# Kernel tuning notes

Measured on AMD Instinct MI355X. Metric: run time of the kernel, lower is better.

The kernel has to match this reference:

```python
import jax, jax.numpy as jnp
import numpy as np

N_NODES = 50000
N_EDGES = 1600000
IN_FEAT = 256
OUT_FEAT = 64


def setup_inputs() -> dict:
    key = jax.random.key(0)
    k1, k2, k3, k4, k5, k6 = jax.random.split(key, 6)
    feat = jax.random.normal(k1, (N_NODES, IN_FEAT), dtype=jnp.float32)
    edge_src = jax.random.randint(k2, (N_EDGES,), 0, N_NODES, dtype=jnp.int32)
    edge_dst = jax.random.randint(k3, (N_EDGES,), 0, N_NODES, dtype=jnp.int32)
    edge_weight = jax.random.uniform(k4, (N_EDGES,), dtype=jnp.float32)
    # Xavier-uniform init as in reset_parameters
    bound = float(np.sqrt(6.0 / (IN_FEAT + OUT_FEAT)))
    W_self = jax.random.uniform(k5, (IN_FEAT, OUT_FEAT), minval=-bound, maxval=bound, dtype=jnp.float32)
    W_neigh = jax.random.uniform(k6, (IN_FEAT, OUT_FEAT), minval=-bound, maxval=bound, dtype=jnp.float32)
    return {"feat": feat, "edge_src": edge_src, "edge_dst": edge_dst,
            "edge_weight": edge_weight, "W_self": W_self, "W_neigh": W_neigh}


def reference(feat, edge_src, edge_dst, edge_weight, W_self, W_neigh):
    # neigh_feat = spmm(adj, feat): row dst aggregates weighted neighbors src
    gathered = feat[edge_src] * edge_weight[:, None]          # [E, in_feat]
    neigh_feat = jax.ops.segment_sum(gathered, edge_dst, num_segments=N_NODES)  # [N, in_feat]
    self_feat = feat @ W_self                                 # [N, out_feat]
    neigh_feat = neigh_feat @ W_neigh                         # [N, out_feat]
    out = jax.nn.relu(self_feat + neigh_feat)
    # dropout p=0.0 -> identity
    return out
```

## Files before the change

### kernel.cpp

```cpp
#include <hip/hip_runtime.h>

#define IN_FEAT 256
#define OUT_FEAT 64
#define BBITS 5
#define BSZ 32
#define CAP_SLICE 256
#define CAP_BUCKET 1600
#define CNT_STRIDE 16

typedef __attribute__((ext_vector_type(8))) short bf16x8;
typedef __attribute__((ext_vector_type(4))) float f32x4;

static __device__ __forceinline__ short f2bf(float f) {
    unsigned u = __float_as_uint(f);
    unsigned r = (u + 0x7FFFu + ((u >> 16) & 1u)) >> 16;
    return (short)r;
}
static __device__ __forceinline__ float bflo(unsigned v) {
    return __uint_as_float(v << 16);
}
static __device__ __forceinline__ float bfhi(unsigned v) {
    return __uint_as_float(v & 0xFFFF0000u);
}

__global__ __launch_bounds__(256) void prep(
    const float* __restrict__ Wself,
    const float* __restrict__ Wneigh,
    bf16x8* __restrict__ Wfrag,
    int* __restrict__ cnt, int cnt_words)
{
    const int t = blockIdx.x * 256 + threadIdx.x;
    if (t < 4096) {
        const int kstep = t >> 9;
        const int ntile = (t >> 6) & 7;
        const int lane  = t & 63;
        const int quad  = lane >> 4;
        const int n     = ntile * 16 + (lane & 15);
        const float* src = (n < OUT_FEAT) ? (Wself + n) : (Wneigh + (n - OUT_FEAT));
        const int k0 = kstep * 32 + quad * 8;
        bf16x8 v;
#pragma unroll
        for (int j = 0; j < 8; ++j) v[j] = f2bf(src[(size_t)(k0 + j) * OUT_FEAT]);
        Wfrag[t] = v;
    }
    const int nthr = gridDim.x * 256;
    for (int i = t; i < cnt_words; i += nthr) cnt[i] = 0;
}

__global__ __launch_bounds__(256) void gemm_scatter(
    const float* __restrict__ feat,
    const bf16x8* __restrict__ Wfrag,
    unsigned short* __restrict__ accSelf,
    unsigned short* __restrict__ Pn,
    const int* __restrict__ esrc,
    const int* __restrict__ edst,
    const float* __restrict__ ew,
    int* __restrict__ cnt,
    unsigned* __restrict__ binned,
    int n_nodes, int n_edges, int NB)
{
    const int wave = threadIdx.x >> 6;
    const int lane = threadIdx.x & 63;

    if (wave == 0) {
        const int row0 = blockIdx.x * 16;
        if (row0 < n_nodes) {
            const int quad = lane >> 4;
            const int l15  = lane & 15;

            f32x4 c[8];
#pragma unroll
            for (int i = 0; i < 8; ++i) c[i] = (f32x4){0.f, 0.f, 0.f, 0.f};

            const int arow = min(row0 + l15, n_nodes - 1);
            const float* afeat = feat + (size_t)arow * IN_FEAT + quad * 8;

#pragma unroll
            for (int kstep = 0; kstep < 8; ++kstep) {
                const float4 x = *(const float4*)(afeat + kstep * 32);
                const float4 y = *(const float4*)(afeat + kstep * 32 + 4);
                bf16x8 a;
                a[0] = f2bf(x.x); a[1] = f2bf(x.y); a[2] = f2bf(x.z); a[3] = f2bf(x.w);
                a[4] = f2bf(y.x); a[5] = f2bf(y.y); a[6] = f2bf(y.z); a[7] = f2bf(y.w);
                bf16x8 b[8];
#pragma unroll
                for (int nt = 0; nt < 8; ++nt) b[nt] = Wfrag[(kstep * 8 + nt) * 64 + lane];
#pragma unroll
                for (int nt = 0; nt < 8; ++nt)
                    c[nt] = __builtin_amdgcn_mfma_f32_16x16x32_bf16(a, b[nt], c[nt], 0, 0, 0);
            }

#pragma unroll
            for (int nt = 0; nt < 8; ++nt) {
                unsigned short* dst = (nt < 4) ? accSelf : Pn;
                const int col = (nt & 3) * 16 + l15;
#pragma unroll
                for (int r = 0; r < 4; ++r) {
                    const int row = row0 + quad * 4 + r;
                    if (row < n_nodes)
                        dst[(size_t)row * OUT_FEAT + col] = (unsigned short)f2bf(c[nt][r]);
                }
            }
        }
    }

    {
        const long base  = (long)blockIdx.x * 512;
        const int slice = blockIdx.x & 7;
        int bin[2], pos[2];
        unsigned rec[2];
        bool ok[2];
#pragma unroll
        for (int k = 0; k < 2; ++k) {
            const long idx = base + k * 256 + (int)threadIdx.x;
            ok[k] = idx < n_edges;
            if (ok[k]) {
                const int d = edst[idx];
                const unsigned s  = (unsigned)esrc[idx];
                const unsigned wq = (unsigned)__float2int_rn(ew[idx] * 2047.0f);
                bin[k] = d >> BBITS;
                rec[k] = ((unsigned)(d & (BSZ - 1)) << 27) | (wq << 16) | s;
            }
        }
#pragma unroll
        for (int k = 0; k < 2; ++k)
            if (ok[k]) pos[k] = atomicAdd(&cnt[((size_t)slice * NB + bin[k]) * CNT_STRIDE], 1);
#pragma unroll
        for (int k = 0; k < 2; ++k)
            if (ok[k] && pos[k] < CAP_SLICE)
                binned[((size_t)slice * NB + bin[k]) * CAP_SLICE + pos[k]] = rec[k];
    }
}

__global__ __launch_bounds__(256) void bucket_gather(
    const unsigned* __restrict__ binned,
    const int* __restrict__ cnt,
    const unsigned short* __restrict__ Pn,
    const unsigned short* __restrict__ accSelf,
    float* __restrict__ out, int n_nodes, int NB)
{
    __shared__ unsigned raw[8 * CAP_SLICE];
    __shared__ int2 sepk[CAP_BUCKET];
    __shared__ int  scnt[8];
    __shared__ int  hcnt[BSZ];
    __shared__ int  hoff[BSZ + 1];
    __shared__ int  hcur[BSZ];

    const int b = blockIdx.x;
    const int t = threadIdx.x;

    if (t < 8) scnt[t] = min(cnt[((size_t)t * NB + b) * CNT_STRIDE], CAP_SLICE);
    if (t < BSZ) hcnt[t] = 0;
    __syncthreads();

#pragma unroll
    for (int sl = 0; sl < 8; ++sl) {
        const int nrec  = scnt[sl];
        const int nrec4 = (nrec + 3) >> 2;
        const uint4* rb4 = (const uint4*)(binned + ((size_t)sl * NB + b) * CAP_SLICE);
        uint4* rw4 = (uint4*)(raw + sl * CAP_SLICE);
        for (int i = t; i < nrec4; i += 256) {
            const uint4 v = rb4[i];
            rw4[i] = v;
            const int e0 = i * 4;
            if (e0 + 0 < nrec) atomicAdd(&hcnt[v.x >> 27], 1);
            if (e0 + 1 < nrec) atomicAdd(&hcnt[v.y >> 27], 1);
            if (e0 + 2 < nrec) atomicAdd(&hcnt[v.z >> 27], 1);
            if (e0 + 3 < nrec) atomicAdd(&hcnt[v.w >> 27], 1);
        }
    }
    __syncthreads();
    if (t == 0) {
        int run = 0;
#pragma unroll
        for (int k = 0; k < BSZ; ++k) { hoff[k] = run; run += hcnt[k]; }
        hoff[BSZ] = run;
    }
    __syncthreads();
    if (t < BSZ) hcur[t] = hoff[t];
    __syncthreads();

#pragma unroll
    for (int sl = 0; sl < 8; ++sl) {
        const int nrec = scnt[sl];
        const unsigned* rw = raw + sl * CAP_SLICE;
        for (int i = t; i < nrec; i += 256) {
            const unsigned p = rw[i];
            const int pos = atomicAdd(&hcur[p >> 27], 1);
            if (pos < CAP_BUCKET) {
                const float w = (float)((p >> 16) & 0x7FFu) * (1.0f / 2047.0f);
                sepk[pos] = make_int2((int)(p & 0xFFFFu), __float_as_int(w));
            }
        }
    }
    __syncthreads();

    const int wv   = t >> 6;
    const int lane = t & 63;
    const int half = lane >> 5;
    const int c2   = (lane & 31) * 2;

#pragma unroll
    for (int ldn = wv * 8; ldn < wv * 8 + 8; ++ldn) {
        const int dst = b * BSZ + ldn;
        if (dst >= n_nodes) break;
        const int beg = min(hoff[ldn], CAP_BUCKET);
        const int end = min(hoff[ldn + 1], CAP_BUCKET);

        float A0[8], A1[8];
#pragma unroll
        for (int j = 0; j < 8; ++j) { A0[j] = 0.f; A1[j] = 0.f; }

        int e = beg + half;
        for (; e + 14 < end; e += 16) {
#pragma unroll
            for (int j = 0; j < 8; ++j) {
                const int2 p = sepk[e + 2 * j];
                const unsigned v = *(const unsigned*)(Pn + (size_t)p.x * OUT_FEAT + c2);
                const float w = __int_as_float(p.y);
                A0[j] += w * bflo(v);
                A1[j] += w * bfhi(v);
            }
        }
        for (; e + 6 < end; e += 8) {
#pragma unroll
            for (int j = 0; j < 4; ++j) {
                const int2 p = sepk[e + 2 * j];
                const unsigned v = *(const unsigned*)(Pn + (size_t)p.x * OUT_FEAT + c2);
                const float w = __int_as_float(p.y);
                A0[j] += w * bflo(v);
                A1[j] += w * bfhi(v);
            }
        }
        for (; e < end; e += 2) {
            const int2 p = sepk[e];
            const unsigned v = *(const unsigned*)(Pn + (size_t)p.x * OUT_FEAT + c2);
            const float w = __int_as_float(p.y);
            A0[0] += w * bflo(v);
            A1[0] += w * bfhi(v);
        }
        float s0 = ((A0[0] + A0[1]) + (A0[2] + A0[3])) + ((A0[4] + A0[5]) + (A0[6] + A0[7]));
        float s1 = ((A1[0] + A1[1]) + (A1[2] + A1[3])) + ((A1[4] + A1[5]) + (A1[6] + A1[7]));
        s0 += __shfl_xor(s0, 32, 64);
        s1 += __shfl_xor(s1, 32, 64);
        if (half == 0) {
            const unsigned sv = *(const unsigned*)(accSelf + (size_t)dst * OUT_FEAT + c2);
            float2 o;
            o.x = fmaxf(bflo(sv) + s0, 0.f);
            o.y = fmaxf(bfhi(sv) + s1, 0.f);
            *(float2*)(out + (size_t)dst * OUT_FEAT + c2) = o;
        }
    }
}

extern "C" void kernel_launch(void* const* d_in, const int* in_sizes, int n_in,
                              void* d_out, int out_size, void* d_ws, size_t ws_size,
                              hipStream_t stream) {
    const float* feat   = (const float*)d_in[0];
    const int*   esrc   = (const int*)  d_in[1];
    const int*   edst   = (const int*)  d_in[2];
    const float* ew     = (const float*)d_in[3];
    const float* Wself  = (const float*)d_in[4];
    const float* Wneigh = (const float*)d_in[5];

    const int n_nodes = in_sizes[0] / IN_FEAT;
    const int n_edges = in_sizes[1];
    const int NB = (n_nodes + BSZ - 1) / BSZ;

    bf16x8* Wfrag           = (bf16x8*)d_ws;
    unsigned short* accSelf = (unsigned short*)((char*)d_ws + 65536);
    unsigned short* Pn      = accSelf + (size_t)n_nodes * OUT_FEAT;
    unsigned* binned = (unsigned*)(Pn + (size_t)n_nodes * OUT_FEAT);
    int*   cnt     = (int*)(binned + (size_t)8 * NB * CAP_SLICE);
    float* out     = (float*)d_out;

    const int cnt_words = 8 * NB * CNT_STRIDE;
    prep<<<64, 256, 0, stream>>>(Wself, Wneigh, Wfrag, cnt, cnt_words);

    const int sblocks = (n_edges + 511) / 512;
    const int tblocks = (n_nodes + 15) / 16;
    const int fblocks = (sblocks > tblocks) ? sblocks : tblocks;
    gemm_scatter<<<fblocks, 256, 0, stream>>>(
        feat, Wfrag, accSelf, Pn, esrc, edst, ew, cnt, binned, n_nodes, n_edges, NB);

    bucket_gather<<<NB, 256, 0, stream>>>(binned, cnt, Pn, accSelf, out, n_nodes, NB);
}
```

Baseline: 210.3 us.

## Aggregate edge binning via per-block LDS histogram and single bucket array

The scatter phase now builds a shared-memory histogram of destination buckets for 4096 edges per block, reserves space with one global atomic per nonempty bucket, then places records using LDS atomics. This replaces one global atomic per edge spread across 8 slices. Buckets become one contiguous array of capacity 1280, so the gather kernel copies a single segment instead of 8. The GEMM part now uses all 8 waves of a 512-thread block. The risks are that edges are read twice, there is LDS contention on hot buckets, and records past the capacity limit are dropped silently.

After: 202.6 us. 3.7% less time.

```diff
diff --git a/kernel.cpp b/kernel.cpp
--- a/kernel.cpp
+++ b/kernel.cpp
@@ -4,9 +4,11 @@
 #define OUT_FEAT 64
 #define BBITS 5
 #define BSZ 32
-#define CAP_SLICE 256
-#define CAP_BUCKET 1600
+#define NBMAX 1568
+#define CAPB 1280
 #define CNT_STRIDE 16
+#define EPB 4096
+#define SCT 512
 
 typedef __attribute__((ext_vector_type(8))) short bf16x8;
 typedef __attribute__((ext_vector_type(4))) float f32x4;
@@ -47,7 +49,7 @@
     for (int i = t; i < cnt_words; i += nthr) cnt[i] = 0;
 }
 
-__global__ __launch_bounds__(256) void gemm_scatter(
+__global__ __launch_bounds__(512) void gemm_scatter(
     const float* __restrict__ feat,
     const bf16x8* __restrict__ Wfrag,
     unsigned short* __restrict__ accSelf,
@@ -59,11 +61,17 @@
     unsigned* __restrict__ binned,
     int n_nodes, int n_edges, int NB)
 {
-    const int wave = threadIdx.x >> 6;
-    const int lane = threadIdx.x & 63;
-
-    if (wave == 0) {
-        const int row0 = blockIdx.x * 16;
+    __shared__ int hist[NBMAX];
+    __shared__ int cur[NBMAX];
+
+    const int t    = threadIdx.x;
+    const int wave = t >> 6;
+    const int lane = t & 63;
+
+    for (int i = t; i < NB; i += SCT) hist[i] = 0;
+
+    {
+        const int row0 = (blockIdx.x * 8 + wave) * 16;
         if (row0 < n_nodes) {
             const int quad = lane >> 4;
             const int l15  = lane & 15;
@@ -103,32 +111,34 @@
             }
         }
     }
-
-    {
-        const long base  = (long)blockIdx.x * 512;
-        const int slice = blockIdx.x & 7;
-        int bin[2], pos[2];
-        unsigned rec[2];
-        bool ok[2];
-#pragma unroll
-        for (int k = 0; k < 2; ++k) {
-            const long idx = base + k * 256 + (int)threadIdx.x;
-            ok[k] = idx < n_edges;
-            if (ok[k]) {
-                const int d = edst[idx];
-                const unsigned s  = (unsigned)esrc[idx];
-                const unsigned wq = (unsigned)__float2int_rn(ew[idx] * 2047.0f);
-                bin[k] = d >> BBITS;
-                rec[k] = ((unsigned)(d & (BSZ - 1)) << 27) | (wq << 16) | s;
-            }
-        }
-#pragma unroll
-        for (int k = 0; k < 2; ++k)
-            if (ok[k]) pos[k] = atomicAdd(&cnt[((size_t)slice * NB + bin[k]) * CNT_STRIDE], 1);
-#pragma unroll
-        for (int k = 0; k < 2; ++k)
-            if (ok[k] && pos[k] < CAP_SLICE)
-                binned[((size_t)slice * NB + bin[k]) * CAP_SLICE + pos[k]] = rec[k];
+    __syncthreads();
+
+    const long base = (long)blockIdx.x * EPB;
+#pragma unroll
+    for (int k = 0; k < 8; ++k) {
+        const long idx = base + k * SCT + t;
+        if (idx < n_edges) atomicAdd(&hist[edst[idx] >> BBITS], 1);
+    }
+    __syncthreads();
+
+    for (int i = t; i < NB; i += SCT) {
+        const int h = hist[i];
+        cur[i] = h ? atomicAdd(&cnt[(size_t)i * CNT_STRIDE], h) : 0;
+    }
+    __syncthreads();
+
+#pragma unroll
+    for (int k = 0; k < 8; ++k) {
+        const long idx = base + k * SCT + t;
+        if (idx < n_edges) {
+            const int d = edst[idx];
+            const unsigned s  = (unsigned)esrc[idx];
+            const unsigned wq = (unsigned)__float2int_rn(ew[idx] * 2047.0f);
+            const unsigned rec = ((unsigned)(d & (BSZ - 1)) << 27) | (wq << 16) | s;
+            const int b = d >> BBITS;
+            const int slot = atomicAdd(&cur[b], 1);
+            if (slot < CAPB) binned[(size_t)b * CAPB + slot] = rec;
+        }
     }
 }
 
@@ -139,26 +149,25 @@
     const unsigned short* __restrict__ accSelf,
     float* __restrict__ out, int n_nodes, int NB)
 {
-    __shared__ unsigned raw[8 * CAP_SLICE];
-    __shared__ int2 sepk[CAP_BUCKET];
-    __shared__ int  scnt[8];
+    __shared__ unsigned raw[CAPB];
+    __shared__ int2 sepk[CAPB];
     __shared__ int  hcnt[BSZ];
     __shared__ int  hoff[BSZ + 1];
     __shared__ int  hcur[BSZ];
+    __shared__ int  snrec;
 
     const int b = blockIdx.x;
     const int t = threadIdx.x;
 
-    if (t < 8) scnt[t] = min(cnt[((size_t)t * NB + b) * CNT_STRIDE], CAP_SLICE);
+    if (t == 0) snrec = min(cnt[(size_t)b * CNT_STRIDE], CAPB);
     if (t < BSZ) hcnt[t] = 0;
     __syncthreads();
-
-#pragma unroll
-    for (int sl = 0; sl < 8; ++sl) {
-        const int nrec  = scnt[sl];
-        const int nrec4 = (nrec + 3) >> 2;
-        const uint4* rb4 = (const uint4*)(binned + ((size_t)sl * NB + b) * CAP_SLICE);
-        uint4* rw4 = (uint4*)(raw + sl * CAP_SLICE);
+    const int nrec  = snrec;
+    const int nrec4 = (nrec + 3) >> 2;
+
+    {
+        const uint4* rb4 = (const uint4*)(binned + (size_t)b * CAPB);
+        uint4* rw4 = (uint4*)raw;
         for (int i = t; i < nrec4; i += 256) {
             const uint4 v = rb4[i];
             rw4[i] = v;
@@ -180,18 +189,11 @@
     if (t < BSZ) hcur[t] = hoff[t];
     __syncthreads();
 
-#pragma unroll
-    for (int sl = 0; sl < 8; ++sl) {
-        const int nrec = scnt[sl];
-        const unsigned* rw = raw + sl * CAP_SLICE;
-        for (int i = t; i < nrec; i += 256) {
-            const unsigned p = rw[i];
-            const int pos = atomicAdd(&hcur[p >> 27], 1);
-            if (pos < CAP_BUCKET) {
-                const float w = (float)((p >> 16) & 0x7FFu) * (1.0f / 2047.0f);
-                sepk[pos] = make_int2((int)(p & 0xFFFFu), __float_as_int(w));
-            }
-        }
+    for (int i = t; i < nrec; i += 256) {
+        const unsigned p = raw[i];
+        const int pos = atomicAdd(&hcur[p >> 27], 1);
+        const float w = (float)((p >> 16) & 0x7FFu) * (1.0f / 2047.0f);
+        sepk[pos] = make_int2((int)(p & 0xFFFFu), __float_as_int(w));
     }
     __syncthreads();
 
@@ -204,8 +206,8 @@
     for (int ldn = wv * 8; ldn < wv * 8 + 8; ++ldn) {
         const int dst = b * BSZ + ldn;
         if (dst >= n_nodes) break;
-        const int beg = min(hoff[ldn], CAP_BUCKET);
-        const int end = min(hoff[ldn + 1], CAP_BUCKET);
+        const int beg = hoff[ldn];
+        const int end = hoff[ldn + 1];
 
         float A0[8], A1[8];
 #pragma unroll
@@ -271,16 +273,16 @@
     unsigned short* accSelf = (unsigned short*)((char*)d_ws + 65536);
     unsigned short* Pn      = accSelf + (size_t)n_nodes * OUT_FEAT;
     unsigned* binned = (unsigned*)(Pn + (size_t)n_nodes * OUT_FEAT);
-    int*   cnt     = (int*)(binned + (size_t)8 * NB * CAP_SLICE);
+    int*   cnt     = (int*)(binned + (size_t)NB * CAPB);
     float* out     = (float*)d_out;
 
-    const int cnt_words = 8 * NB * CNT_STRIDE;
+    const int cnt_words = NB * CNT_STRIDE;
     prep<<<64, 256, 0, stream>>>(Wself, Wneigh, Wfrag, cnt, cnt_words);
 
-    const int sblocks = (n_edges + 511) / 512;
-    const int tblocks = (n_nodes + 15) / 16;
+    const int sblocks = (n_edges + EPB - 1) / EPB;
+    const int tblocks = (((n_nodes + 15) / 16) + 7) / 8;
     const int fblocks = (sblocks > tblocks) ? sblocks : tblocks;
-    gemm_scatter<<<fblocks, 256, 0, stream>>>(
+    gemm_scatter<<<fblocks, SCT, 0, stream>>>(
         feat, Wfrag, accSelf, Pn, esrc, edst, ew, cnt, binned, n_nodes, n_edges, NB);
 
     bucket_gather<<<NB, 256, 0, stream>>>(binned, cnt, Pn, accSelf, out, n_nodes, NB);
```

## Aggregate edge binning atomics through shared-memory histogram per block

Applied to the files above, without the earlier changes.

Each block now handles 2048 edges. It builds a block-local histogram of destination buckets in LDS, then issues one global atomicAdd per nonempty bucket to reserve a range, and assigns each edge's slot with LDS atomics. The GEMM part also uses all four waves, each taking 16 rows, so fewer blocks are launched. This is meant to cut global atomic traffic and contention. In exchange it adds barriers, 12.5KB of LDS per block, and a second read of esrc and ew. With NBMAX fixed at 1568, the LDS arrays overflow if there are more than about 50k nodes.

Measured after the change: 204.5 us. -2.7%, faster.

```diff
diff --git a/kernel.cpp b/kernel.cpp
--- a/kernel.cpp
+++ b/kernel.cpp
@@ -4,9 +4,12 @@
 #define OUT_FEAT 64
 #define BBITS 5
 #define BSZ 32
+#define NBMAX 1568
 #define CAP_SLICE 256
 #define CAP_BUCKET 1600
 #define CNT_STRIDE 16
+#define EPB 2048
+#define SCT 256
 
 typedef __attribute__((ext_vector_type(8))) short bf16x8;
 typedef __attribute__((ext_vector_type(4))) float f32x4;
@@ -47,7 +50,7 @@
     for (int i = t; i < cnt_words; i += nthr) cnt[i] = 0;
 }
 
-__global__ __launch_bounds__(256) void gemm_scatter(
+__global__ __launch_bounds__(SCT) void gemm_scatter(
     const float* __restrict__ feat,
     const bf16x8* __restrict__ Wfrag,
     unsigned short* __restrict__ accSelf,
@@ -59,11 +62,18 @@
     unsigned* __restrict__ binned,
     int n_nodes, int n_edges, int NB)
 {
-    const int wave = threadIdx.x >> 6;
-    const int lane = threadIdx.x & 63;
-
-    if (wave == 0) {
-        const int row0 = blockIdx.x * 16;
+    __shared__ int hist[NBMAX];
+    __shared__ int cur[NBMAX];
+
+    const int t    = threadIdx.x;
+    const int wave = t >> 6;
+    const int lane = t & 63;
+    const int slice = blockIdx.x & 7;
+
+    for (int i = t; i < NB; i += SCT) hist[i] = 0;
+
+    {
+        const int row0 = (blockIdx.x * 4 + wave) * 16;
         if (row0 < n_nodes) {
             const int quad = lane >> 4;
             const int l15  = lane & 15;
@@ -103,32 +113,39 @@
             }
         }
     }
-
-    {
-        const long base  = (long)blockIdx.x * 512;
-        const int slice = blockIdx.x & 7;
-        int bin[2], pos[2];
-        unsigned rec[2];
-        bool ok[2];
-#pragma unroll
-        for (int k = 0; k < 2; ++k) {
-            const long idx = base + k * 256 + (int)threadIdx.x;
-            ok[k] = idx < n_edges;
-            if (ok[k]) {
-                const int d = edst[idx];
-                const unsigned s  = (unsigned)esrc[idx];
-                const unsigned wq = (unsigned)__float2int_rn(ew[idx] * 2047.0f);
-                bin[k] = d >> BBITS;
-                rec[k] = ((unsigned)(d & (BSZ - 1)) << 27) | (wq << 16) | s;
-            }
-        }
-#pragma unroll
-        for (int k = 0; k < 2; ++k)
-            if (ok[k]) pos[k] = atomicAdd(&cnt[((size_t)slice * NB + bin[k]) * CNT_STRIDE], 1);
-#pragma unroll
-        for (int k = 0; k < 2; ++k)
-            if (ok[k] && pos[k] < CAP_SLICE)
-                binned[((size_t)slice * NB + bin[k]) * CAP_SLICE + pos[k]] = rec[k];
+    __syncthreads();
+
+    const long base = (long)blockIdx.x * EPB;
+    int d[8];
+    bool ok[8];
+#pragma unroll
+    for (int k = 0; k < 8; ++k) {
+        const long idx = base + k * SCT + t;
+        ok[k] = idx < n_edges;
+        if (ok[k]) {
+            d[k] = edst[idx];
+            atomicAdd(&hist[d[k] >> BBITS], 1);
+        }
+    }
+    __syncthreads();
+
+    for (int i = t; i < NB; i += SCT) {
+        const int h = hist[i];
+        cur[i] = h ? atomicAdd(&cnt[((size_t)slice * NB + i) * CNT_STRIDE], h) : 0;
+    }
+    __syncthreads();
+
+#pragma unroll
+    for (int k = 0; k < 8; ++k) {
+        if (ok[k]) {
+            const long idx = base + k * SCT + t;
+            const unsigned s  = (unsigned)esrc[idx];
+            const unsigned wq = (unsigned)__float2int_rn(ew[idx] * 2047.0f);
+            const unsigned rec = ((unsigned)(d[k] & (BSZ - 1)) << 27) | (wq << 16) | s;
+            const int b = d[k] >> BBITS;
+            const int slot = atomicAdd(&cur[b], 1);
+            if (slot < CAP_SLICE) binned[((size_t)slice * NB + b) * CAP_SLICE + slot] = rec;
+        }
     }
 }
 
@@ -277,10 +294,10 @@
     const int cnt_words = 8 * NB * CNT_STRIDE;
     prep<<<64, 256, 0, stream>>>(Wself, Wneigh, Wfrag, cnt, cnt_words);
 
-    const int sblocks = (n_edges + 511) / 512;
-    const int tblocks = (n_nodes + 15) / 16;
+    const int sblocks = (n_edges + EPB - 1) / EPB;
+    const int tblocks = (((n_nodes + 15) / 16) + 3) / 4;
     const int fblocks = (sblocks > tblocks) ? sblocks : tblocks;
-    gemm_scatter<<<fblocks, 256, 0, stream>>>(
+    gemm_scatter<<<fblocks, SCT, 0, stream>>>(
         feat, Wfrag, accSelf, Pn, esrc, edst, ew, cnt, binned, n_nodes, n_edges, NB);
 
     bucket_gather<<<NB, 256, 0, stream>>>(binned, cnt, Pn, accSelf, out, n_nodes, NB);
```
